# Optimization experiments

Measured on AMD Instinct MI355X. Metric: run time of the kernel, lower is better.

Reference implementation:

```python
import jax, jax.numpy as jnp
import numpy as np

B, S, K, N = 8, 8192, 1024, 1024  # batch, seq, in_features, out_features

def setup_inputs() -> dict:
    key = jax.random.key(0)
    k1, k2, k3, k4 = jax.random.split(key, 4)
    x = jax.random.normal(k1, (B, S, K), dtype=jnp.float32)
    # int8 codes stored as float (matches fp16 CB parameter in the module)
    CB = jnp.clip(jnp.round(jax.random.normal(k2, (N, K), dtype=jnp.float32) * 42.0), -127.0, 127.0)
    # per-output-channel absmax scales (positive)
    SCB = jax.random.uniform(k3, (N,), dtype=jnp.float32, minval=0.5, maxval=2.0)
    bias = jax.random.normal(k4, (N,), dtype=jnp.float32) * 0.02
    return {"x": x, "CB": CB, "SCB": SCB, "bias": bias}

def reference(x, CB, SCB, bias):
    # out = linear(x, CB) * (SCB/127) + bias  -- scale applied AFTER the GEMM,
    # exactly as in the non-BFA forward path of my_8bit_linear.
    out = jnp.einsum('bsk,nk->bsn', x, CB)        # [B, S, N]
    out = out * (SCB * (1.0 / 127.0)) + bias      # per-output-channel dequant + bias
    return out
```

## Files before the change

kernel.cpp:

```cpp
#include <hip/hip_runtime.h>

typedef _Float16 half8 __attribute__((ext_vector_type(8)));
typedef _Float16 half4 __attribute__((ext_vector_type(4)));
typedef float    f32x4 __attribute__((ext_vector_type(4)));

constexpr int Mtot = 65536;
constexpr int Ntot = 1024;
constexpr int Ktot = 1024;

constexpr int BM = 128, BN = 128, BK = 32;
constexpr int KT = Ktot / BK;

__global__ __launch_bounds__(256, 2)
void q8lin_gemm_kernel(const float* __restrict__ X,
                       const float* __restrict__ CB,
                       const float* __restrict__ SCB,
                       const float* __restrict__ BIAS,
                       float* __restrict__ OUT)
{
    __shared__ _Float16 As[2][BM][BK];
    __shared__ _Float16 Bs[2][BN][BK];

    const int nwg   = gridDim.x;
    const int chunk = nwg >> 3;
    const int bid   = blockIdx.x;
    const int wg    = (bid & 7) * chunk + (bid >> 3);

    const int ntile = wg & 7;
    const int mtile = wg >> 3;
    const int brow  = mtile * BM;
    const int bcol  = ntile * BN;

    const int tid  = threadIdx.x;
    const int lane = tid & 63;
    const int wid  = tid >> 6;
    const int wm   = wid >> 1;
    const int wn   = wid & 1;

    const float* aBase = X  + brow * Ktot;
    const float* bBase = CB + bcol * Ktot;

    const int c4 = tid & 7;
    const int r0 = tid >> 3;

    f32x4 acc[4][4];
#pragma unroll
    for (int m = 0; m < 4; ++m)
#pragma unroll
        for (int n = 0; n < 4; ++n)
            acc[m][n] = (f32x4)0.0f;

    float4 arg[4], brg[4];

    auto loadTiles = [&](int t) {
        const float* ap = aBase + t * BK + c4 * 4;
        const float* bp = bBase + t * BK + c4 * 4;
#pragma unroll
        for (int s = 0; s < 4; ++s) {
            const int row = r0 + s * 32;
            arg[s] = *(const float4*)(ap + row * Ktot);
            brg[s] = *(const float4*)(bp + row * Ktot);
        }
    };

    auto writeTiles = [&](int buf) {
#pragma unroll
        for (int s = 0; s < 4; ++s) {
            const int row = r0 + s * 32;
            half4 ha = { (_Float16)arg[s].x, (_Float16)arg[s].y,
                         (_Float16)arg[s].z, (_Float16)arg[s].w };
            half4 hb = { (_Float16)brg[s].x, (_Float16)brg[s].y,
                         (_Float16)brg[s].z, (_Float16)brg[s].w };
            *(half4*)&As[buf][row][c4 * 4] = ha;
            *(half4*)&Bs[buf][row][c4 * 4] = hb;
        }
    };

    loadTiles(0);
    writeTiles(0);
    __syncthreads();

    const int rA = lane & 15;
    const int ko = (lane >> 4) * 8;

    for (int t = 0; t < KT; ++t) {
        const int cur = t & 1;

        if (t + 1 < KT) loadTiles(t + 1);

        half8 af[4], bf[4];
#pragma unroll
        for (int m = 0; m < 4; ++m)
            af[m] = *(const half8*)&As[cur][wm * 64 + m * 16 + rA][ko];
#pragma unroll
        for (int n = 0; n < 4; ++n)
            bf[n] = *(const half8*)&Bs[cur][wn * 64 + n * 16 + rA][ko];

#pragma unroll
        for (int m = 0; m < 4; ++m)
#pragma unroll
            for (int n = 0; n < 4; ++n)
                acc[m][n] = __builtin_amdgcn_mfma_f32_16x16x32_f16(
                    af[m], bf[n], acc[m][n], 0, 0, 0);

        if (t + 1 < KT) writeTiles(cur ^ 1);
        __syncthreads();
    }

    const float inv127 = 1.0f / 127.0f;
#pragma unroll
    for (int n = 0; n < 4; ++n) {
        const int col = bcol + wn * 64 + n * 16 + rA;
        const float s  = SCB[col] * inv127;
        const float bb = BIAS[col];
#pragma unroll
        for (int m = 0; m < 4; ++m) {
            const int grow = brow + wm * 64 + m * 16 + ((lane >> 4) << 2);
            float* op = OUT + grow * Ntot + col;
#pragma unroll
            for (int j = 0; j < 4; ++j)
                op[j * Ntot] = acc[m][n][j] * s + bb;
        }
    }
}

extern "C" void kernel_launch(void* const* d_in, const int* in_sizes, int n_in,
                              void* d_out, int out_size, void* d_ws, size_t ws_size,
                              hipStream_t stream) {
    const float* X    = (const float*)d_in[0];
    const float* CB   = (const float*)d_in[1];
    const float* SCB  = (const float*)d_in[2];
    const float* BIAS = (const float*)d_in[3];
    float* OUT = (float*)d_out;

    const int grid = (Mtot / BM) * (Ntot / BN);
    q8lin_gemm_kernel<<<dim3(grid), dim3(256), 0, stream>>>(X, CB, SCB, BIAS, OUT);
}
```

Baseline: 695.5 us.

## Pre-pack inputs to swizzled fp16 and run 256x256 GEMM with direct-to-LDS loads

Adds a conversion pass that casts X and CB to fp16 in a tiled, XOR-swizzled layout in workspace. The main GEMM then uses 256x256x64 tiles with 512 threads, global_load_lds asynchronous copies, a four-phase software pipeline with explicit vmcnt waits and setprio. This removes the in-loop fp32-to-fp16 conversion and register staging, and halves the GEMM's A-operand bytes. The cost is an extra full read of X (fp32) plus a write of its fp16 copy. A fallback kernel with padded LDS runs when the workspace is too small.

```diff
diff --git a/kernel.cpp b/kernel.cpp
--- a/kernel.cpp
+++ b/kernel.cpp
@@ -4,65 +4,192 @@
 typedef _Float16 half4 __attribute__((ext_vector_type(4)));
 typedef float    f32x4 __attribute__((ext_vector_type(4)));
 
-constexpr int Mtot = 65536;
-constexpr int Ntot = 1024;
-constexpr int Ktot = 1024;
-
-constexpr int BM = 128, BN = 128, BK = 32;
+constexpr int Mtot = 65536, Ntot = 1024, Ktot = 1024;
+constexpr int BM = 256, BN = 256, BK = 64;
 constexpr int KT = Ktot / BK;
-
-__global__ __launch_bounds__(256, 2)
-void q8lin_gemm_kernel(const float* __restrict__ X,
-                       const float* __restrict__ CB,
-                       const float* __restrict__ SCB,
-                       const float* __restrict__ BIAS,
-                       float* __restrict__ OUT)
+constexpr int MT = Mtot / BM;
+constexpr int NT = Ntot / BN;
+
+constexpr size_t XH_BYTES  = (size_t)MT * KT * 2 * 1024 * 16;
+constexpr size_t CBH_BYTES = (size_t)NT * KT * 2 * 1024 * 16;
+
+__global__ __launch_bounds__(256)
+void cvt_pack(const float* __restrict__ src, _Float16* __restrict__ dst)
 {
-    __shared__ _Float16 As[2][BM][BK];
-    __shared__ _Float16 Bs[2][BN][BK];
-
-    const int nwg   = gridDim.x;
-    const int chunk = nwg >> 3;
-    const int bid   = blockIdx.x;
-    const int wg    = (bid & 7) * chunk + (bid >> 3);
-
-    const int ntile = wg & 7;
-    const int mtile = wg >> 3;
-    const int brow  = mtile * BM;
-    const int bcol  = ntile * BN;
+    const int C     = blockIdx.x * 256 + threadIdx.x;
+    const int tile  = C >> 15;
+    const int rem   = C & 32767;
+    const int kt    = rem >> 11;
+    const int kh    = (rem >> 10) & 1;
+    const int off16 = rem & 1023;
+    const int r     = off16 >> 2;
+    const int hi    = (off16 & 3) ^ ((r >> 1) & 3);
+    const float* s  = src + (size_t)(tile * 256 + r) * Ktot + kt * 64 + kh * 32 + hi * 8;
+    f32x4 a = *(const f32x4*)s;
+    f32x4 b = *(const f32x4*)(s + 4);
+    half8 h = { (_Float16)a[0], (_Float16)a[1], (_Float16)a[2], (_Float16)a[3],
+                (_Float16)b[0], (_Float16)b[1], (_Float16)b[2], (_Float16)b[3] };
+    *(half8*)(dst + (size_t)C * 8) = h;
+}
+
+__global__ __launch_bounds__(512, 2)
+void gemm8(const _Float16* __restrict__ Xh, const _Float16* __restrict__ CBh,
+           const float* __restrict__ SCB,  const float* __restrict__ BIAS,
+           float* __restrict__ OUT)
+{
+    __shared__ __align__(16) _Float16 lds[65536];
+
+    const int nwg = gridDim.x;
+    const int bid = blockIdx.x;
+    const int wg  = (bid & 7) * (nwg >> 3) + (bid >> 3);
+    const int nt  = wg & 3;
+    const int mt  = wg >> 2;
+    const int brow = mt * BM;
+    const int bcol = nt * BN;
 
     const int tid  = threadIdx.x;
     const int lane = tid & 63;
     const int wid  = tid >> 6;
-    const int wm   = wid >> 1;
-    const int wn   = wid & 1;
-
-    const float* aBase = X  + brow * Ktot;
-    const float* bBase = CB + bcol * Ktot;
-
-    const int c4 = tid & 7;
-    const int r0 = tid >> 3;
-
-    f32x4 acc[4][4];
-#pragma unroll
-    for (int m = 0; m < 4; ++m)
+    const int wm   = wid >> 2;
+    const int wn   = wid & 3;
+    const int rA   = lane & 15;
+    const int hi   = lane >> 4;
+    const int sl   = hi ^ ((rA >> 1) & 3);
+
+    const int aBaseH = (wm * 128 + rA) * 32 + sl * 8;
+    const int bBaseH = 32768 + (wn * 64 + rA) * 32 + sl * 8;
+
+    f32x4 acc[8][4];
+#pragma unroll
+    for (int m = 0; m < 8; ++m)
 #pragma unroll
         for (int n = 0; n < 4; ++n)
             acc[m][n] = (f32x4)0.0f;
 
+    auto stageA = [&](int kt, int kh, int buf) {
+        const _Float16* sp = Xh + (size_t)((mt * KT + kt) * 2 + kh) * 8192;
+#pragma unroll
+        for (int g = 0; g < 2; ++g) {
+            const int cell = g * 512 + tid;
+            __builtin_amdgcn_global_load_lds(
+                (const __attribute__((address_space(1))) void*)(sp + (size_t)cell * 8),
+                (__attribute__((address_space(3))) void*)(&lds[buf * 16384 + kh * 8192 + cell * 8]),
+                16, 0, 0);
+        }
+    };
+    auto stageB = [&](int kt, int kh, int buf) {
+        const _Float16* sp = CBh + (size_t)((nt * KT + kt) * 2 + kh) * 8192;
+#pragma unroll
+        for (int g = 0; g < 2; ++g) {
+            const int cell = g * 512 + tid;
+            __builtin_amdgcn_global_load_lds(
+                (const __attribute__((address_space(1))) void*)(sp + (size_t)cell * 8),
+                (__attribute__((address_space(3))) void*)(&lds[32768 + buf * 16384 + kh * 8192 + cell * 8]),
+                16, 0, 0);
+        }
+    };
+
+    auto phase = [&](int c, int ks, int mh, auto&& stageFn, int vm) {
+        half8 af[4], bf[4];
+        const int ab = c * 16384 + ks * 8192;
+#pragma unroll
+        for (int f = 0; f < 4; ++f)
+            af[f] = *(const half8*)&lds[ab + aBaseH + mh * 2048 + f * 512];
+#pragma unroll
+        for (int n = 0; n < 4; ++n)
+            bf[n] = *(const half8*)&lds[ab + bBaseH + n * 512];
+        stageFn();
+        __builtin_amdgcn_s_barrier();
+        __builtin_amdgcn_s_setprio(1);
+#pragma unroll
+        for (int f = 0; f < 4; ++f)
+#pragma unroll
+            for (int n = 0; n < 4; ++n)
+                acc[mh * 4 + f][n] = __builtin_amdgcn_mfma_f32_16x16x32_f16(
+                    af[f], bf[n], acc[mh * 4 + f][n], 0, 0, 0);
+        __builtin_amdgcn_s_setprio(0);
+        if (vm == 4)      asm volatile("s_waitcnt vmcnt(4)" ::: "memory");
+        else if (vm == 0) asm volatile("s_waitcnt vmcnt(0)" ::: "memory");
+        __builtin_amdgcn_s_barrier();
+        __builtin_amdgcn_sched_barrier(0);
+    };
+
+    stageA(0, 0, 0); stageB(0, 0, 0);
+    stageA(0, 1, 0); stageB(0, 1, 0);
+    asm volatile("s_waitcnt vmcnt(4)" ::: "memory");
+    __builtin_amdgcn_s_barrier();
+    __builtin_amdgcn_sched_barrier(0);
+
+    for (int t = 0; t < KT - 1; ++t) {
+        const int c = t & 1, nb = c ^ 1;
+        phase(c, 0, 0, [&] { stageA(t + 1, 0, nb); }, -1);
+        phase(c, 0, 1, [&] { stageB(t + 1, 0, nb); },  4);
+        phase(c, 1, 0, [&] { stageA(t + 1, 1, nb); }, -1);
+        phase(c, 1, 1, [&] { stageB(t + 1, 1, nb); },  4);
+    }
+    phase(1, 0, 0, [] {}, -1);
+    phase(1, 0, 1, [] {},  0);
+    phase(1, 1, 0, [] {}, -1);
+    phase(1, 1, 1, [] {}, -1);
+
+    const float inv127 = 1.0f / 127.0f;
+#pragma unroll
+    for (int n = 0; n < 4; ++n) {
+        const int col = bcol + wn * 64 + n * 16 + rA;
+        const float s  = SCB[col] * inv127;
+        const float bb = BIAS[col];
+#pragma unroll
+        for (int m = 0; m < 8; ++m) {
+            const int grow = brow + wm * 128 + m * 16 + (hi << 2);
+            float* op = OUT + (size_t)grow * Ntot + col;
+#pragma unroll
+            for (int j = 0; j < 4; ++j)
+                op[(size_t)j * Ntot] = acc[m][n][j] * s + bb;
+        }
+    }
+}
+
+namespace fb {
+constexpr int BMf = 128, BNf = 128, BKf = 32;
+constexpr int KTf = Ktot / BKf;
+constexpr int LDK = 40;
+
+__global__ __launch_bounds__(256, 2)
+void gemm_fb(const float* __restrict__ X, const float* __restrict__ CB,
+             const float* __restrict__ SCB, const float* __restrict__ BIAS,
+             float* __restrict__ OUT)
+{
+    __shared__ _Float16 As[2][BMf][LDK];
+    __shared__ _Float16 Bs[2][BNf][LDK];
+
+    const int nwg = gridDim.x;
+    const int bid = blockIdx.x;
+    const int wg  = (bid & 7) * (nwg >> 3) + (bid >> 3);
+    const int ntile = wg & 7;
+    const int mtile = wg >> 3;
+    const int brow = mtile * BMf;
+    const int bcol = ntile * BNf;
+
+    const int tid = threadIdx.x, lane = tid & 63, wid = tid >> 6;
+    const int wm = wid >> 1, wn = wid & 1;
+    const int c4 = tid & 7, r0 = tid >> 3;
+    const float* aBase = X  + (size_t)(brow + r0) * Ktot + c4 * 4;
+    const float* bBase = CB + (size_t)(bcol + r0) * Ktot + c4 * 4;
+
+    f32x4 acc[4][4];
+#pragma unroll
+    for (int m = 0; m < 4; ++m)
+#pragma unroll
+        for (int n = 0; n < 4; ++n) acc[m][n] = (f32x4)0.0f;
+
     float4 arg[4], brg[4];
-
     auto loadTiles = [&](int t) {
-        const float* ap = aBase + t * BK + c4 * 4;
-        const float* bp = bBase + t * BK + c4 * 4;
 #pragma unroll
         for (int s = 0; s < 4; ++s) {
-            const int row = r0 + s * 32;
-            arg[s] = *(const float4*)(ap + row * Ktot);
-            brg[s] = *(const float4*)(bp + row * Ktot);
-        }
-    };
-
+            arg[s] = *(const float4*)(aBase + (size_t)s * 32 * Ktot + t * BKf);
+            brg[s] = *(const float4*)(bBase + (size_t)s * 32 * Ktot + t * BKf);
+        }
+    };
     auto writeTiles = [&](int buf) {
 #pragma unroll
         for (int s = 0; s < 4; ++s) {
@@ -76,34 +203,24 @@
         }
     };
 
-    loadTiles(0);
-    writeTiles(0);
+    loadTiles(0); writeTiles(0); loadTiles(1);
     __syncthreads();
-
-    const int rA = lane & 15;
-    const int ko = (lane >> 4) * 8;
-
-    for (int t = 0; t < KT; ++t) {
+    const int rA = lane & 15, ko = (lane >> 4) * 8;
+
+    for (int t = 0; t < KTf; ++t) {
         const int cur = t & 1;
-
-        if (t + 1 < KT) loadTiles(t + 1);
-
+        if (t + 1 < KTf) writeTiles(cur ^ 1);
+        if (t + 2 < KTf) loadTiles(t + 2);
         half8 af[4], bf[4];
 #pragma unroll
+        for (int m = 0; m < 4; ++m) af[m] = *(const half8*)&As[cur][wm * 64 + m * 16 + rA][ko];
+#pragma unroll
+        for (int n = 0; n < 4; ++n) bf[n] = *(const half8*)&Bs[cur][wn * 64 + n * 16 + rA][ko];
+#pragma unroll
         for (int m = 0; m < 4; ++m)
-            af[m] = *(const half8*)&As[cur][wm * 64 + m * 16 + rA][ko];
-#pragma unroll
-        for (int n = 0; n < 4; ++n)
-            bf[n] = *(const half8*)&Bs[cur][wn * 64 + n * 16 + rA][ko];
-
-#pragma unroll
-        for (int m = 0; m < 4; ++m)
 #pragma unroll
             for (int n = 0; n < 4; ++n)
-                acc[m][n] = __builtin_amdgcn_mfma_f32_16x16x32_f16(
-                    af[m], bf[n], acc[m][n], 0, 0, 0);
-
-        if (t + 1 < KT) writeTiles(cur ^ 1);
+                acc[m][n] = __builtin_amdgcn_mfma_f32_16x16x32_f16(af[m], bf[n], acc[m][n], 0, 0, 0);
         __syncthreads();
     }
 
@@ -111,17 +228,17 @@
 #pragma unroll
     for (int n = 0; n < 4; ++n) {
         const int col = bcol + wn * 64 + n * 16 + rA;
-        const float s  = SCB[col] * inv127;
+        const float s = SCB[col] * inv127;
         const float bb = BIAS[col];
 #pragma unroll
         for (int m = 0; m < 4; ++m) {
             const int grow = brow + wm * 64 + m * 16 + ((lane >> 4) << 2);
-            float* op = OUT + grow * Ntot + col;
-#pragma unroll
-            for (int j = 0; j < 4; ++j)
-                op[j * Ntot] = acc[m][n][j] * s + bb;
-        }
-    }
+            float* op = OUT + (size_t)grow * Ntot + col;
+#pragma unroll
+            for (int j = 0; j < 4; ++j) op[(size_t)j * Ntot] = acc[m][n][j] * s + bb;
+        }
+    }
+}
 }
 
 extern "C" void kernel_launch(void* const* d_in, const int* in_sizes, int n_in,
@@ -133,6 +250,15 @@
     const float* BIAS = (const float*)d_in[3];
     float* OUT = (float*)d_out;
 
-    const int grid = (Mtot / BM) * (Ntot / BN);
-    q8lin_gemm_kernel<<<dim3(grid), dim3(256), 0, stream>>>(X, CB, SCB, BIAS, OUT);
-}
+    if (ws_size < XH_BYTES + CBH_BYTES) {
+        fb::gemm_fb<<<dim3(4096), dim3(256), 0, stream>>>(X, CB, SCB, BIAS, OUT);
+        return;
+    }
+
+    _Float16* Xh  = (_Float16*)d_ws;
+    _Float16* CBh = (_Float16*)((char*)d_ws + XH_BYTES);
+
+    cvt_pack<<<dim3(32768), dim3(256), 0, stream>>>(X, Xh);
+    cvt_pack<<<dim3(512),   dim3(256), 0, stream>>>(CB, CBh);
+    gemm8<<<dim3(MT * NT), dim3(512), 0, stream>>>(Xh, CBh, SCB, BIAS, OUT);
+}
```

New measurement: 584.3 us. 1.19x faster.
